# Kernel optimization log

Measured on AMD Instinct MI355X. Metric: run time of the kernel, lower is better.

The kernel has to match this reference:

```python
import jax, jax.numpy as jnp
import numpy as np

NUM_HEADS = 4

def _pos_encoding(seq_len, d, dtype):
    # standard sinusoidal positional encoding [seq_len, d]
    pos = jnp.arange(seq_len, dtype=jnp.float32)[:, None]
    i = jnp.arange(0, d, 2, dtype=jnp.float32)
    div = jnp.exp(-jnp.log(10000.0) * i / d)
    ang = pos * div
    pe = jnp.zeros((seq_len, d), jnp.float32)
    pe = pe.at[:, 0::2].set(jnp.sin(ang)).at[:, 1::2].set(jnp.cos(ang))
    return pe.astype(dtype)

def _layer_norm(x, g, b, eps=1e-5):
    m = jnp.mean(x, axis=-1, keepdims=True)
    v = jnp.mean(jnp.square(x - m), axis=-1, keepdims=True)
    return (x - m) / jnp.sqrt(v + eps) * g + b

def setup_inputs() -> dict:
    key = jax.random.key(0)
    ks = jax.random.split(key, 10)
    B, S, H, W, N = 8, 512, 768, 8, 4096
    s = 0.02
    token_reps = jax.random.normal(ks[0], (B, S, H), jnp.float32)
    starts = jax.random.randint(ks[1], (B, N), 0, S - W)
    widths = jax.random.randint(ks[2], (B, N), 1, W + 1)
    span_ids = jnp.stack([starts, starts + widths], axis=-1)  # end > start, end <= S
    span_masks = jax.random.randint(ks[3], (B, N), 0, 2)
    return dict(
        token_reps=token_reps,
        dummy_query=jax.random.normal(ks[4], (H,), jnp.float32) * s,
        in_proj_w=jax.random.normal(ks[5], (3 * H, H), jnp.float32) * s,
        in_proj_b=jnp.zeros((3 * H,), jnp.float32),
        out_w=jax.random.normal(ks[6], (H, H), jnp.float32) * s,
        out_b=jnp.zeros((H,), jnp.float32),
        ln_g=jnp.ones((H,), jnp.float32),
        ln_b=jnp.zeros((H,), jnp.float32),
        ffn_w1=jax.random.normal(ks[7], (H, 4 * H), jnp.float32) * s,
        ffn_b1=jnp.zeros((4 * H,), jnp.float32),
        ffn_w2=jax.random.normal(ks[8], (4 * H, H), jnp.float32) * s,
        ffn_b2=jnp.zeros((H,), jnp.float32),
        span_ids=span_ids,
        span_masks=span_masks,
    )

def reference(token_reps, dummy_query, in_proj_w, in_proj_b, out_w, out_b,
              ln_g, ln_b, ffn_w1, ffn_b1, ffn_w2, ffn_b2, span_ids, span_masks):
    B, S, H = token_reps.shape
    N = span_ids.shape[1]
    NH = NUM_HEADS
    DH = H // NH
    # sequence positional encoding (dropout is identity in eval mode)
    x = token_reps + _pos_encoding(S, H, token_reps.dtype)[None]
    Wq, Wk, Wv = jnp.split(in_proj_w, 3, axis=0)
    bq, bk, bv = jnp.split(in_proj_b, 3)
    # single shared dummy query -> per-head query [NH, DH]
    q = (dummy_query @ Wq.T + bq).reshape(NH, DH)
    k = (x @ Wk.T + bk).reshape(B, S, NH, DH)
    v = (x @ Wv.T + bv).reshape(B, S, NH, DH)
    # scores are identical across spans since the query is shared: [B, NH, S]
    scores = jnp.einsum('hd,bshd->bhs', q, k) / jnp.sqrt(jnp.asarray(DH, x.dtype))
    pos = jnp.arange(S)
    # per-span key validity: start <= pos < end, and span not masked out  [B, N, S]
    valid = (pos[None, None, :] >= span_ids[..., 0:1]) & \
            (pos[None, None, :] < span_ids[..., 1:2]) & \
            (span_masks[..., None] != 0)
    logits = jnp.where(valid[:, :, None, :], scores[:, None, :, :], -1e9)  # [B,N,NH,S]
    w = jax.nn.softmax(logits, axis=-1)
    attn = jnp.einsum('bnhs,bshd->bnhd', w, v).reshape(B, N, H)
    attn = attn @ out_w.T + out_b
    h1 = _layer_norm(attn + dummy_query, ln_g, ln_b)
    ffn = jax.nn.relu(h1 @ ffn_w1 + ffn_b1) @ ffn_w2 + ffn_b2
    out = _layer_norm(ffn + h1, ln_g, ln_b)
    # masked spans produce exact zeros, matching the original loop
    return out * (span_masks[..., None] != 0).astype(out.dtype)
```

## Files before the change

kernel.cpp:

```cpp
#include <hip/hip_runtime.h>
#include <hip/hip_bf16.h>

#define Bb 8
#define Ss 512
#define Hh 768
#define NHh 4
#define Nn 4096
#define ROWS (Bb * Nn)
#define SCB 128

typedef _Float16 f16x8 __attribute__((ext_vector_type(8)));
typedef _Float16 f16x4 __attribute__((ext_vector_type(4)));
typedef _Float16 f16x2 __attribute__((ext_vector_type(2)));
typedef float f32x4 __attribute__((ext_vector_type(4)));

#define DEVINL __device__ __forceinline__

DEVINL void gld_lds16(const void* g, void* l) {
  __builtin_amdgcn_global_load_lds(
      (const __attribute__((address_space(1))) void*)g,
      (__attribute__((address_space(3))) void*)l, 16, 0, 0);
}

template <int V>
DEVINL void wait_vmcnt() {
  if constexpr (V == 0) asm volatile("s_waitcnt vmcnt(0)" ::: "memory");
  else if constexpr (V == 3) asm volatile("s_waitcnt vmcnt(3)" ::: "memory");
  else if constexpr (V == 4) asm volatile("s_waitcnt vmcnt(4)" ::: "memory");
  else if constexpr (V == 6) asm volatile("s_waitcnt vmcnt(6)" ::: "memory");
  else if constexpr (V == 8) asm volatile("s_waitcnt vmcnt(8)" ::: "memory");
}

DEVINL float block_sum256(float v, float* red) {
#pragma unroll
  for (int o = 32; o; o >>= 1) v += __shfl_xor(v, o, 64);
  const int wid = threadIdx.x >> 6, lane = threadIdx.x & 63;
  if (lane == 0) red[wid] = v;
  __syncthreads();
  float r = red[0] + red[1] + red[2] + red[3];
  __syncthreads();
  return r;
}

__global__ __launch_bounds__(256) void x_kernel(const float* __restrict__ tok,
                                                _Float16* __restrict__ x) {
  int idx = blockIdx.x * 256 + threadIdx.x;
  int t = idx % 384;
  int bs = idx / 384;
  int s = bs & (Ss - 1);
  float div = expf(-(float)t * 0.02398526138535465f);
  float ang = (float)s * div;
  float sv = sinf(ang), cv = cosf(ang);
  const float2 tv = ((const float2*)tok)[(size_t)bs * 384 + t];
  f16x2 o;
  o[0] = (_Float16)(tv.x + sv);
  o[1] = (_Float16)(tv.y + cv);
  *(f16x2*)&x[(size_t)bs * Hh + 2 * t] = o;
}

__global__ __launch_bounds__(256) void q_kernel(const float* __restrict__ dq,
                                                const float* __restrict__ ipw,
                                                const float* __restrict__ ipb,
                                                float* __restrict__ qout) {
  __shared__ float red[4];
  int o = blockIdx.x;
  const float* wr = ipw + (size_t)o * Hh;
  float s = 0.f;
#pragma unroll
  for (int e = 0; e < 3; e++) {
    int j = threadIdx.x + 256 * e;
    s += dq[j] * wr[j];
  }
  s = block_sum256(s, red);
  if (threadIdx.x == 0) qout[o] = s + ipb[o];
}

__global__ __launch_bounds__(256) void c_kernel(const float* __restrict__ q,
                                                const float* __restrict__ ipw,
                                                const float* __restrict__ ipb,
                                                float* __restrict__ cout,
                                                float* __restrict__ sbias) {
  __shared__ float red[4];
  int bid = blockIdx.x;
  int t = threadIdx.x;
  if (bid < 3072) {
    int h = bid / Hh;
    int j = bid - h * Hh;
    float s = 0.f;
    if (t < 192) s = q[h * 192 + t] * ipw[(size_t)(Hh + h * 192 + t) * Hh + j];
    s = block_sum256(s, red);
    if (t == 0) cout[bid] = s;
  } else {
    int h = bid - 3072;
    float s = 0.f;
    if (t < 192) s = q[h * 192 + t] * ipb[Hh + h * 192 + t];
    s = block_sum256(s, red);
    if (t == 0) sbias[h] = s;
  }
}

__global__ __launch_bounds__(256) void score_kernel(
    const _Float16* __restrict__ x, const float* __restrict__ c,
    const float* __restrict__ sbias, float* __restrict__ scores) {
  int bs = blockIdx.x;
  int wid = threadIdx.x >> 6, lane = threadIdx.x & 63;
  const _Float16* xr = x + (size_t)bs * Hh;
  const float* ch = c + wid * Hh;
  float s = 0.f;
#pragma unroll
  for (int e = 0; e < 12; e++) {
    int j = e * 64 + lane;
    s += (float)xr[j] * ch[j];
  }
#pragma unroll
  for (int o = 32; o; o >>= 1) s += __shfl_xor(s, o, 64);
  if (lane == 0) {
    int b = bs >> 9, pos = bs & (Ss - 1);
    scores[((size_t)(b * NHh + wid)) * Ss + pos] =
        (s + sbias[wid]) * 0.07216878364870322f;
  }
}

__global__ __launch_bounds__(256) void cvt_kernel(const float* __restrict__ in,
                                                  _Float16* __restrict__ out) {
  int i = blockIdx.x * 256 + threadIdx.x;
  float4 f = ((const float4*)in)[i];
  f16x4 o;
  o[0] = (_Float16)f.x;
  o[1] = (_Float16)f.y;
  o[2] = (_Float16)f.z;
  o[3] = (_Float16)f.w;
  ((f16x4*)out)[i] = o;
}

__global__ __launch_bounds__(256) void trcvt_kernel(const float* __restrict__ in,
                                                    _Float16* __restrict__ out,
                                                    int R, int C) {
  __shared__ float tile[32][33];
  int c0 = blockIdx.x * 32, r0 = blockIdx.y * 32;
  int tx = threadIdx.x & 31, ty0 = threadIdx.x >> 5;
#pragma unroll
  for (int ty = ty0; ty < 32; ty += 8)
    tile[ty][tx] = in[(size_t)(r0 + ty) * C + c0 + tx];
  __syncthreads();
#pragma unroll
  for (int ty = ty0; ty < 32; ty += 8)
    out[(size_t)(c0 + ty) * R + r0 + tx] = (_Float16)tile[tx][ty];
}

__global__ __launch_bounds__(256) void scan1_kernel(const int* __restrict__ mask,
                                                    int* __restrict__ bsum) {
  int r = blockIdx.x * 256 + threadIdx.x;
  unsigned long long b = __ballot(mask[r] != 0);
  __shared__ int wsum[4];
  int lane = threadIdx.x & 63, wid = threadIdx.x >> 6;
  if (lane == 0) wsum[wid] = __popcll(b);
  __syncthreads();
  if (threadIdx.x == 0)
    bsum[blockIdx.x] = wsum[0] + wsum[1] + wsum[2] + wsum[3];
}
__global__ __launch_bounds__(64) void scan2_kernel(const int* __restrict__ bsum,
                                                   int* __restrict__ boff,
                                                   int* __restrict__ cnt) {
  if (threadIdx.x == 0) {
    int acc = 0;
    for (int i = 0; i < SCB; i++) {
      boff[i] = acc;
      acc += bsum[i];
    }
    *cnt = acc;
  }
}
__global__ __launch_bounds__(256) void cidx_kernel(const int* __restrict__ mask,
                                                   const int* __restrict__ boff,
                                                   int* __restrict__ cidx) {
  int r = blockIdx.x * 256 + threadIdx.x;
  int m = mask[r] != 0;
  unsigned long long b = __ballot(m);
  __shared__ int wsum[4];
  int lane = threadIdx.x & 63, wid = threadIdx.x >> 6;
  if (lane == 0) wsum[wid] = __popcll(b);
  __syncthreads();
  int pre = 0;
#pragma unroll
  for (int i = 0; i < 3; i++)
    if (i < wid) pre += wsum[i];
  pre += __popcll(b & ((1ULL << lane) - 1));
  if (m) cidx[r] = boff[blockIdx.x] + pre;
}

template <int RELU, int BN>
__global__ __launch_bounds__(256, 2) void gemm_nt(
    const _Float16* __restrict__ A, const _Float16* __restrict__ W,
    const float* __restrict__ bias, _Float16* __restrict__ C, int N, int K,
    int nn, const int* __restrict__ mcount) {
  const int bid = (int)blockIdx.x;
  const int mi = (bid >> 3) / nn;
  const int nt_ = (bid >> 3) - mi * nn;
  const long m0 = (long)(mi * 8 + (bid & 7)) * 128;
  const long n0 = (long)nt_ * BN;
  if (mcount && m0 >= (long)*mcount) return;
  __shared__ __align__(16) _Float16 As[3][128 * 32];
  __shared__ __align__(16) _Float16 Bs[3][BN * 32];
  const int tid = threadIdx.x;
  const int wid = tid >> 6;
  const int lane = tid & 63;
  constexpr int LPS = (BN == 128) ? 4 : 3;

  const int c0 = wid * 64 + lane;
  const int c1 = c0 + 256;
  const int sw0 = ((c0 & 3) ^ ((c0 >> 3) & 3)) * 8;
  const int sw1 = ((c1 & 3) ^ ((c1 >> 3) & 3)) * 8;
  const _Float16* gA0 = A + (m0 + (c0 >> 2)) * K + sw0;
  const _Float16* gA1 = A + (m0 + (c1 >> 2)) * K + sw1;
  const _Float16* gB0 = W + (n0 + (c0 >> 2)) * K + sw0;
  const _Float16* gB1 = W + (n0 + (c1 >> 2)) * K + sw1;

  const int wr = (wid >> 1) * 64;
  const int wc = (wid & 1) * (BN / 2);
  constexpr int NF = BN / 32;
  const int fr = lane & 15;
  const int fkb = lane >> 4;

  f32x4 acc[4][NF];
#pragma unroll
  for (int mi2 = 0; mi2 < 4; mi2++)
#pragma unroll
    for (int ni = 0; ni < NF; ni++) acc[mi2][ni] = (f32x4){0.f, 0.f, 0.f, 0.f};

#define STAGE(buf, k0)                                                  \
  do {                                                                  \
    gld_lds16(gA0 + (k0), &As[buf][wid * 512]);                         \
    gld_lds16(gA1 + (k0), &As[buf][2048 + wid * 512]);                  \
    gld_lds16(gB0 + (k0), &Bs[buf][wid * 512]);                         \
    if constexpr (BN == 128) gld_lds16(gB1 + (k0), &Bs[buf][2048 + wid * 512]); \
  } while (0)

#define COMPUTE(buf)                                                          \
  do {                                                                        \
    f16x8 af[4], bf[NF];                                                      \
    _Pragma("unroll") for (int i = 0; i < 4; i++) {                           \
      int r_ = wr + i * 16 + fr;                                              \
      af[i] = *(const f16x8*)&As[buf][r_ * 32 + ((fkb ^ ((r_ >> 1) & 3)) * 8)]; \
    }                                                                         \
    _Pragma("unroll") for (int i = 0; i < NF; i++) {                          \
      int r_ = wc + i * 16 + fr;                                              \
      bf[i] = *(const f16x8*)&Bs[buf][r_ * 32 + ((fkb ^ ((r_ >> 1) & 3)) * 8)]; \
    }                                                                         \
    __builtin_amdgcn_s_setprio(1);                                            \
    _Pragma("unroll") for (int mi2 = 0; mi2 < 4; mi2++)                       \
        _Pragma("unroll") for (int ni = 0; ni < NF; ni++)                     \
            acc[mi2][ni] = __builtin_amdgcn_mfma_f32_16x16x32_f16(            \
                af[mi2], bf[ni], acc[mi2][ni], 0, 0, 0);                      \
    __builtin_amdgcn_s_setprio(0);                                            \
  } while (0)

#define ITER_RESTAGE(b, knext)              \
  do {                                      \
    wait_vmcnt<2 * LPS>();                  \
    __builtin_amdgcn_s_barrier();           \
    COMPUTE(b);                             \
    __builtin_amdgcn_s_barrier();           \
    STAGE(b, (knext));                      \
  } while (0)

  const int nt = K >> 5;
  STAGE(0, 0);
  STAGE(1, 32);
  STAGE(2, 64);
  int t = 0;
  for (; t <= nt - 6; t += 3) {
    ITER_RESTAGE(0, (t + 3) * 32);
    ITER_RESTAGE(1, (t + 4) * 32);
    ITER_RESTAGE(2, (t + 5) * 32);
  }
  wait_vmcnt<2 * LPS>();
  __builtin_amdgcn_s_barrier();
  COMPUTE(0);
  wait_vmcnt<LPS>();
  __builtin_amdgcn_s_barrier();
  COMPUTE(1);
  wait_vmcnt<0>();
  __builtin_amdgcn_s_barrier();
  COMPUTE(2);
#undef STAGE
#undef COMPUTE
#undef ITER_RESTAGE

  const int crow = (lane >> 4) * 4;
  const int ccol = lane & 15;
  float bv[NF];
#pragma unroll
  for (int ni = 0; ni < NF; ni++)
    bv[ni] = bias ? bias[n0 + wc + ni * 16 + ccol] : 0.f;
#pragma unroll
  for (int mi2 = 0; mi2 < 4; mi2++)
#pragma unroll
    for (int ni = 0; ni < NF; ni++)
#pragma unroll
      for (int i = 0; i < 4; i++) {
        float v = acc[mi2][ni][i] + bv[ni];
        if (RELU) v = fmaxf(v, 0.f);
        C[(m0 + wr + mi2 * 16 + crow + i) * (long)N + (n0 + wc + ni * 16 + ccol)] =
            (_Float16)v;
      }
}

template <int RELU>
__global__ __launch_bounds__(512, 4) void gemm8_nt(
    const _Float16* __restrict__ A, const _Float16* __restrict__ W,
    const float* __restrict__ bias, _Float16* __restrict__ C, int N, int K,
    int nn, const int* __restrict__ mcount) {
  const int bid = (int)blockIdx.x;
  const int mi = (bid >> 3) / nn;
  const int nt_ = (bid >> 3) - mi * nn;
  const long m0 = (long)(mi * 8 + (bid & 7)) * 256;
  const long n0 = (long)nt_ * 128;
  if (mcount && m0 >= (long)*mcount) return;
  __shared__ __align__(16) _Float16 As[3][256 * 32];
  __shared__ __align__(16) _Float16 Bs[3][128 * 32];
  const int tid = threadIdx.x;
  const int w = tid >> 6;
  const int lane = tid & 63;
  constexpr int LPS = 3;

  const int rA0 = w * 16 + (lane >> 2);
  const int rA1 = rA0 + 128;
  const int cb = lane & 3;
  const int swA0 = (cb ^ ((rA0 >> 1) & 3)) * 8;
  const int swA1 = (cb ^ ((rA1 >> 1) & 3)) * 8;
  const _Float16* gA0 = A + (m0 + rA0) * K + swA0;
  const _Float16* gA1 = A + (m0 + rA1) * K + swA1;
  const _Float16* gB0 = W + (n0 + rA0) * K + swA0;

  const int wr = (w >> 1) * 64;
  const int wc = (w & 1) * 64;
  const int fr = lane & 15;
  const int fkb = lane >> 4;

  f32x4 acc[4][4];
#pragma unroll
  for (int mi2 = 0; mi2 < 4; mi2++)
#pragma unroll
    for (int ni = 0; ni < 4; ni++) acc[mi2][ni] = (f32x4){0.f, 0.f, 0.f, 0.f};

#define STAGE(buf, k0)                                   \
  do {                                                   \
    gld_lds16(gA0 + (k0), &As[buf][w * 512]);            \
    gld_lds16(gA1 + (k0), &As[buf][(w + 8) * 512]);      \
    gld_lds16(gB0 + (k0), &Bs[buf][w * 512]);            \
  } while (0)

#define COMPUTE(buf)                                                          \
  do {                                                                        \
    f16x8 af[4], bf[4];                                                       \
    _Pragma("unroll") for (int i = 0; i < 4; i++) {                           \
      int r_ = wr + i * 16 + fr;                                              \
      af[i] = *(const f16x8*)&As[buf][r_ * 32 + ((fkb ^ ((r_ >> 1) & 3)) * 8)]; \
    }                                                                         \
    _Pragma("unroll") for (int i = 0; i < 4; i++) {                           \
      int r_ = wc + i * 16 + fr;                                              \
      bf[i] = *(const f16x8*)&Bs[buf][r_ * 32 + ((fkb ^ ((r_ >> 1) & 3)) * 8)]; \
    }                                                                         \
    __builtin_amdgcn_s_setprio(1);                                            \
    _Pragma("unroll") for (int mi2 = 0; mi2 < 4; mi2++)                       \
        _Pragma("unroll") for (int ni = 0; ni < 4; ni++)                      \
            acc[mi2][ni] = __builtin_amdgcn_mfma_f32_16x16x32_f16(            \
                af[mi2], bf[ni], acc[mi2][ni], 0, 0, 0);                      \
    __builtin_amdgcn_s_setprio(0);                                            \
  } while (0)

#define ITER_RESTAGE(b, knext)              \
  do {                                      \
    wait_vmcnt<2 * LPS>();                  \
    __builtin_amdgcn_s_barrier();           \
    COMPUTE(b);                             \
    __builtin_amdgcn_s_barrier();           \
    STAGE(b, (knext));                      \
  } while (0)

  const int nt = K >> 5;
  STAGE(0, 0);
  STAGE(1, 32);
  STAGE(2, 64);
  int t = 0;
  for (; t <= nt - 6; t += 3) {
    ITER_RESTAGE(0, (t + 3) * 32);
    ITER_RESTAGE(1, (t + 4) * 32);
    ITER_RESTAGE(2, (t + 5) * 32);
  }
  wait_vmcnt<2 * LPS>();
  __builtin_amdgcn_s_barrier();
  COMPUTE(0);
  wait_vmcnt<LPS>();
  __builtin_amdgcn_s_barrier();
  COMPUTE(1);
  wait_vmcnt<0>();
  __builtin_amdgcn_s_barrier();
  COMPUTE(2);
#undef STAGE
#undef COMPUTE
#undef ITER_RESTAGE

  const int crow = (lane >> 4) * 4;
  const int ccol = lane & 15;
  float bv[4];
#pragma unroll
  for (int ni = 0; ni < 4; ni++)
    bv[ni] = bias ? bias[n0 + wc + ni * 16 + ccol] : 0.f;
#pragma unroll
  for (int mi2 = 0; mi2 < 4; mi2++)
#pragma unroll
    for (int ni = 0; ni < 4; ni++)
#pragma unroll
      for (int i = 0; i < 4; i++) {
        float v = acc[mi2][ni][i] + bv[ni];
        if (RELU) v = fmaxf(v, 0.f);
        C[(m0 + wr + mi2 * 16 + crow + i) * (long)N + (n0 + wc + ni * 16 + ccol)] =
            (_Float16)v;
      }
}

__global__ __launch_bounds__(192) void pool_kernel(
    const _Float16* __restrict__ v, const float* __restrict__ scores,
    const int* __restrict__ span_ids, const int* __restrict__ span_masks,
    _Float16* __restrict__ attn, const int* __restrict__ cidx) {
  int r = blockIdx.x;
  if (span_masks[r] == 0) return;
  int slot = cidx[r];
  int i = threadIdx.x;
  int h = i / 48;
  int d0 = i * 4;
  int b = r >> 12;
  int st = span_ids[2 * r], en = span_ids[2 * r + 1];
  int wdt = en - st;
  const float* sc = scores + ((size_t)(b * NHh + h)) * Ss + st;
  float w[8];
  float mx = -1e30f;
#pragma unroll
  for (int j = 0; j < 8; j++) {
    float t = (j < wdt) ? sc[j] : -1e30f;
    w[j] = t;
    mx = fmaxf(mx, t);
  }
  float sum = 0.f;
#pragma unroll
  for (int j = 0; j < 8; j++) {
    float e = (j < wdt) ? expf(w[j] - mx) : 0.f;
    w[j] = e;
    sum += e;
  }
  float inv = 1.f / sum;
  float a0 = 0.f, a1 = 0.f, a2 = 0.f, a3 = 0.f;
#pragma unroll
  for (int j = 0; j < 8; j++) {
    if (j < wdt) {
      f16x4 vv = *(const f16x4*)(v + ((size_t)(b * Ss + st + j)) * Hh + d0);
      float wj = w[j] * inv;
      a0 += wj * (float)vv[0];
      a1 += wj * (float)vv[1];
      a2 += wj * (float)vv[2];
      a3 += wj * (float)vv[3];
    }
  }
  f16x4 o;
  o[0] = (_Float16)a0;
  o[1] = (_Float16)a1;
  o[2] = (_Float16)a2;
  o[3] = (_Float16)a3;
  *(f16x4*)&attn[(size_t)slot * Hh + d0] = o;
}

__global__ __launch_bounds__(256) void ln0_kernel(
    _Float16* __restrict__ X, const float* __restrict__ AddV,
    const float* __restrict__ g, const float* __restrict__ bta,
    const int* __restrict__ mcount) {
  __shared__ float red[4];
  int r = blockIdx.x;
  if (r >= *mcount) return;
  int t = threadIdx.x;
  float xv[3];
#pragma unroll
  for (int e = 0; e < 3; e++) {
    int d = t + 256 * e;
    xv[e] = (float)X[(size_t)r * Hh + d] + AddV[d];
  }
  float s = xv[0] + xv[1] + xv[2];
  s = block_sum256(s, red);
  float mean = s * (1.f / 768.f);
  float vs = 0.f;
#pragma unroll
  for (int e = 0; e < 3; e++) {
    float d = xv[e] - mean;
    vs += d * d;
  }
  vs = block_sum256(vs, red);
  float inv = rsqrtf(vs * (1.f / 768.f) + 1e-5f);
#pragma unroll
  for (int e = 0; e < 3; e++) {
    int d = t + 256 * e;
    X[(size_t)r * Hh + d] = (_Float16)((xv[e] - mean) * inv * g[d] + bta[d]);
  }
}

__global__ __launch_bounds__(256) void ln1_kernel(
    const _Float16* __restrict__ F2c, const _Float16* __restrict__ h1c,
    const int* __restrict__ cidx, const float* __restrict__ g,
    const float* __restrict__ bta, const int* __restrict__ mask,
    float* __restrict__ out) {
  __shared__ float red[4];
  int r = blockIdx.x;
  int t = threadIdx.x;
  float* orow = out + (size_t)r * Hh;
  if (mask[r] == 0) {
#pragma unroll
    for (int e = 0; e < 3; e++) orow[t + 256 * e] = 0.f;
    return;
  }
  int c = cidx[r];
  float xv[3];
#pragma unroll
  for (int e = 0; e < 3; e++) {
    int d = t + 256 * e;
    xv[e] = (float)F2c[(size_t)c * Hh + d] + (float)h1c[(size_t)c * Hh + d];
  }
  float s = xv[0] + xv[1] + xv[2];
  s = block_sum256(s, red);
  float mean = s * (1.f / 768.f);
  float vs = 0.f;
#pragma unroll
  for (int e = 0; e < 3; e++) {
    float d = xv[e] - mean;
    vs += d * d;
  }
  vs = block_sum256(vs, red);
  float inv = rsqrtf(vs * (1.f / 768.f) + 1e-5f);
#pragma unroll
  for (int e = 0; e < 3; e++) {
    int d = t + 256 * e;
    orow[d] = (xv[e] - mean) * inv * g[d] + bta[d];
  }
}

extern "C" void kernel_launch(void* const* d_in, const int* in_sizes, int n_in,
                              void* d_out, int out_size, void* d_ws,
                              size_t ws_size, hipStream_t stream) {
  (void)out_size;
  if (n_in != 14) return;
  if (in_sizes[0] != 3145728 || in_sizes[2] != 1769472 ||
      in_sizes[3] != 2304 || in_sizes[4] != 589824 ||
      in_sizes[8] != 2359296 || in_sizes[9] != 3072 ||
      in_sizes[12] != 65536 || in_sizes[13] != 32768)
    return;

  const float* tok   = (const float*)d_in[0];
  const float* dq    = (const float*)d_in[1];
  const float* ipw   = (const float*)d_in[2];
  const float* ipb   = (const float*)d_in[3];
  const float* outw  = (const float*)d_in[4];
  const float* outb  = (const float*)d_in[5];
  const float* lng   = (const float*)d_in[6];
  const float* lnb   = (const float*)d_in[7];
  const float* w1    = (const float*)d_in[8];
  const float* b1    = (const float*)d_in[9];
  const float* w2    = (const float*)d_in[10];
  const float* b2    = (const float*)d_in[11];
  const int* spid    = (const int*)d_in[12];
  const int* spmask  = (const int*)d_in[13];

  char* ws = (char*)d_ws;
  size_t off = 0;
  auto alloc = [&](size_t bytes) {
    size_t r = off;
    off = (off + bytes + 255) & ~(size_t)255;
    return r;
  };
  _Float16* X16  = (_Float16*)(ws + alloc((size_t)Bb * Ss * Hh * 2));
  float* SC      = (float*)(ws + alloc((size_t)Bb * NHh * Ss * 4));
  float* Q       = (float*)(ws + alloc(768 * 4));
  float* Cc      = (float*)(ws + alloc(3072 * 4));
  float* SB      = (float*)(ws + alloc(4 * 4));
  _Float16* WV16 = (_Float16*)(ws + alloc((size_t)768 * 768 * 2));
  _Float16* OW16 = (_Float16*)(ws + alloc((size_t)768 * 768 * 2));
  _Float16* WT1  = (_Float16*)(ws + alloc((size_t)3072 * 768 * 2));
  _Float16* WT2  = (_Float16*)(ws + alloc((size_t)768 * 3072 * 2));
  _Float16* ATTN = (_Float16*)(ws + alloc((size_t)ROWS * Hh * 2));
  _Float16* PROJ = (_Float16*)(ws + alloc((size_t)ROWS * Hh * 2));
  _Float16* F1   = (_Float16*)(ws + alloc((size_t)ROWS * 3072 * 2));
  if (ws_size < off) return;
  _Float16* F2 = ATTN;

  int* CIDX = (int*)X16;
  int* BSUM = (int*)X16 + ROWS;
  int* BOFF = (int*)X16 + ROWS + SCB;
  int* CNT  = (int*)X16 + ROWS + 2 * SCB;

  _Float16* V16 = (_Float16*)d_out;

  cvt_kernel<<<576, 256, 0, stream>>>(ipw + (size_t)1536 * 768, WV16);
  cvt_kernel<<<576, 256, 0, stream>>>(outw, OW16);
  trcvt_kernel<<<dim3(96, 24), 256, 0, stream>>>(w1, WT1, 768, 3072);
  trcvt_kernel<<<dim3(24, 96), 256, 0, stream>>>(w2, WT2, 3072, 768);

  x_kernel<<<(Bb * Ss * 384) / 256, 256, 0, stream>>>(tok, X16);
  q_kernel<<<768, 256, 0, stream>>>(dq, ipw, ipb, Q);
  c_kernel<<<3076, 256, 0, stream>>>(Q, ipw, ipb, Cc, SB);
  score_kernel<<<Bb * Ss, 256, 0, stream>>>(X16, Cc, SB, SC);
  gemm_nt<0, 64><<<384, 256, 0, stream>>>(X16, WV16, ipb + 1536, V16,
                                          768, 768, 12, nullptr);
  scan1_kernel<<<SCB, 256, 0, stream>>>(spmask, BSUM);
  scan2_kernel<<<1, 64, 0, stream>>>(BSUM, BOFF, CNT);
  cidx_kernel<<<SCB, 256, 0, stream>>>(spmask, BOFF, CIDX);
  pool_kernel<<<ROWS, 192, 0, stream>>>(V16, SC, spid, spmask, ATTN, CIDX);
  gemm8_nt<0><<<768, 512, 0, stream>>>(ATTN, OW16, outb, PROJ,
                                       768, 768, 6, CNT);
  ln0_kernel<<<ROWS, 256, 0, stream>>>(PROJ, dq, lng, lnb, CNT);
  gemm8_nt<1><<<3072, 512, 0, stream>>>(PROJ, WT1, b1, F1,
                                        3072, 768, 24, CNT);
  gemm8_nt<0><<<768, 512, 0, stream>>>(F1, WT2, b2, F2,
                                       768, 3072, 6, CNT);
  ln1_kernel<<<ROWS, 256, 0, stream>>>(F2, PROJ, CIDX, lng, lnb, spmask,
                                       (float*)d_out);
}
```

Measured before the change: 365.6 us.

## Use 256x256-tile triple-buffered MFMA GEMM for the FFN up-projection

Adds a gemm16_nt kernel with 256x256 output tiles per 512-thread block, where each wave computes a 128x64 sub-tile. It uses three LDS stages filled by global_load_lds, XOR-swizzled to avoid bank conflicts. The FFN first GEMM (768->3072 with ReLU) now launches this kernel with half as many blocks instead of gemm8_nt. The larger tile raises arithmetic intensity and cuts redundant A/W loads. In exchange it uses more registers (128 accumulator floats) and 96KB of LDS, which may limit occupancy, and it quantizes the masked row count to 256-row tiles.

```diff
diff --git a/kernel.cpp b/kernel.cpp
--- a/kernel.cpp
+++ b/kernel.cpp
@@ -421,6 +421,123 @@
       }
 }
 
+template <int RELU>
+__global__ __launch_bounds__(512, 2) void gemm16_nt(
+    const _Float16* __restrict__ A, const _Float16* __restrict__ W,
+    const float* __restrict__ bias, _Float16* __restrict__ C, int N, int K,
+    int nn, const int* __restrict__ mcount) {
+  const int bid = (int)blockIdx.x;
+  const int mi = (bid >> 3) / nn;
+  const int nt_ = (bid >> 3) - mi * nn;
+  const long m0 = (long)(mi * 8 + (bid & 7)) * 256;
+  const long n0 = (long)nt_ * 256;
+  if (mcount && m0 >= (long)*mcount) return;
+  __shared__ __align__(16) _Float16 As[3][256 * 32];
+  __shared__ __align__(16) _Float16 Bs[3][256 * 32];
+  const int tid = threadIdx.x;
+  const int w = tid >> 6;
+  const int lane = tid & 63;
+  constexpr int LPS = 4;
+
+  const int r0c = w * 16 + (lane >> 2);
+  const int r1c = r0c + 128;
+  const int cb = lane & 3;
+  const int sw0 = (cb ^ ((r0c >> 1) & 3)) * 8;
+  const int sw1 = (cb ^ ((r1c >> 1) & 3)) * 8;
+  const _Float16* gA0 = A + (m0 + r0c) * K + sw0;
+  const _Float16* gA1 = A + (m0 + r1c) * K + sw1;
+  const _Float16* gB0 = W + (n0 + r0c) * K + sw0;
+  const _Float16* gB1 = W + (n0 + r1c) * K + sw1;
+
+  const int wr = (w >> 2) * 128;
+  const int wc = (w & 3) * 64;
+  const int fr = lane & 15;
+  const int fkb = lane >> 4;
+
+  f32x4 acc[8][4];
+#pragma unroll
+  for (int mi2 = 0; mi2 < 8; mi2++)
+#pragma unroll
+    for (int ni = 0; ni < 4; ni++) acc[mi2][ni] = (f32x4){0.f, 0.f, 0.f, 0.f};
+
+#define STAGE(buf, k0)                                   \
+  do {                                                   \
+    gld_lds16(gA0 + (k0), &As[buf][w * 512]);            \
+    gld_lds16(gA1 + (k0), &As[buf][(w + 8) * 512]);      \
+    gld_lds16(gB0 + (k0), &Bs[buf][w * 512]);            \
+    gld_lds16(gB1 + (k0), &Bs[buf][(w + 8) * 512]);      \
+  } while (0)
+
+#define COMPUTE(buf)                                                          \
+  do {                                                                        \
+    f16x8 af[8], bf[4];                                                       \
+    _Pragma("unroll") for (int i = 0; i < 8; i++) {                           \
+      int r_ = wr + i * 16 + fr;                                              \
+      af[i] = *(const f16x8*)&As[buf][r_ * 32 + ((fkb ^ ((r_ >> 1) & 3)) * 8)]; \
+    }                                                                         \
+    _Pragma("unroll") for (int i = 0; i < 4; i++) {                           \
+      int r_ = wc + i * 16 + fr;                                              \
+      bf[i] = *(const f16x8*)&Bs[buf][r_ * 32 + ((fkb ^ ((r_ >> 1) & 3)) * 8)]; \
+    }                                                                         \
+    __builtin_amdgcn_s_setprio(1);                                            \
+    _Pragma("unroll") for (int mi2 = 0; mi2 < 8; mi2++)                       \
+        _Pragma("unroll") for (int ni = 0; ni < 4; ni++)                      \
+            acc[mi2][ni] = __builtin_amdgcn_mfma_f32_16x16x32_f16(            \
+                af[mi2], bf[ni], acc[mi2][ni], 0, 0, 0);                      \
+    __builtin_amdgcn_s_setprio(0);                                            \
+  } while (0)
+
+#define ITER_RESTAGE(b, knext)              \
+  do {                                      \
+    wait_vmcnt<2 * LPS>();                  \
+    __builtin_amdgcn_s_barrier();           \
+    COMPUTE(b);                             \
+    __builtin_amdgcn_s_barrier();           \
+    STAGE(b, (knext));                      \
+  } while (0)
+
+  const int nt = K >> 5;
+  STAGE(0, 0);
+  STAGE(1, 32);
+  STAGE(2, 64);
+  int t = 0;
+  for (; t <= nt - 6; t += 3) {
+    ITER_RESTAGE(0, (t + 3) * 32);
+    ITER_RESTAGE(1, (t + 4) * 32);
+    ITER_RESTAGE(2, (t + 5) * 32);
+  }
+  wait_vmcnt<2 * LPS>();
+  __builtin_amdgcn_s_barrier();
+  COMPUTE(0);
+  wait_vmcnt<LPS>();
+  __builtin_amdgcn_s_barrier();
+  COMPUTE(1);
+  wait_vmcnt<0>();
+  __builtin_amdgcn_s_barrier();
+  COMPUTE(2);
+#undef STAGE
+#undef COMPUTE
+#undef ITER_RESTAGE
+
+  const int crow = (lane >> 4) * 4;
+  const int ccol = lane & 15;
+  float bv[4];
+#pragma unroll
+  for (int ni = 0; ni < 4; ni++)
+    bv[ni] = bias ? bias[n0 + wc + ni * 16 + ccol] : 0.f;
+#pragma unroll
+  for (int mi2 = 0; mi2 < 8; mi2++)
+#pragma unroll
+    for (int ni = 0; ni < 4; ni++)
+#pragma unroll
+      for (int i = 0; i < 4; i++) {
+        float v = acc[mi2][ni][i] + bv[ni];
+        if (RELU) v = fmaxf(v, 0.f);
+        C[(m0 + wr + mi2 * 16 + crow + i) * (long)N + (n0 + wc + ni * 16 + ccol)] =
+            (_Float16)v;
+      }
+}
+
 __global__ __launch_bounds__(192) void pool_kernel(
     const _Float16* __restrict__ v, const float* __restrict__ scores,
     const int* __restrict__ span_ids, const int* __restrict__ span_masks,
@@ -615,8 +732,8 @@
   gemm8_nt<0><<<768, 512, 0, stream>>>(ATTN, OW16, outb, PROJ,
                                        768, 768, 6, CNT);
   ln0_kernel<<<ROWS, 256, 0, stream>>>(PROJ, dq, lng, lnb, CNT);
-  gemm8_nt<1><<<3072, 512, 0, stream>>>(PROJ, WT1, b1, F1,
-                                        3072, 768, 24, CNT);
+  gemm16_nt<1><<<1536, 512, 0, stream>>>(PROJ, WT1, b1, F1,
+                                         3072, 768, 12, CNT);
   gemm8_nt<0><<<768, 512, 0, stream>>>(F1, WT2, b2, F2,
                                        768, 3072, 6, CNT);
   ln1_kernel<<<ROWS, 256, 0, stream>>>(F2, PROJ, CIDX, lng, lnb, spmask,
```

After: 379.6 us. 1.04x slower.
